# Optimization experiments

Hardware: AMD Instinct MI355X
Metric: run time of the kernel (lower is better)

## Reference

```python
import jax, jax.numpy as jnp
import numpy as np


def _conv(x, w, b=None, stride=1, pad=0, dil=1):
    out = jax.lax.conv_general_dilated(
        x, w, (stride, stride), [(pad, pad), (pad, pad)],
        rhs_dilation=(dil, dil),
        dimension_numbers=('NCHW', 'OIHW', 'NCHW'))
    return out if b is None else out + b[None, :, None, None]


def _sobel_base(out_ch, in_ch, k=3):
    # Exactly mirrors SobelConv2d weight construction (4 directional kernels).
    w = np.zeros((out_ch, in_ch, k, k), np.float32)
    m = k // 2
    for idx in range(out_ch):
        if idx % 4 == 0:
            w[idx, :, 0, :] = -1; w[idx, :, 0, m] = -2
            w[idx, :, -1, :] = 1; w[idx, :, -1, m] = 2
        elif idx % 4 == 1:
            w[idx, :, :, 0] = -1; w[idx, :, m, 0] = -2
            w[idx, :, :, -1] = 1; w[idx, :, m, -1] = 2
        elif idx % 4 == 2:
            w[idx, :, 0, 0] = -2
            for i in range(m + 1):
                w[idx, :, m - i, i] = -1
                w[idx, :, k - 1 - i, m + i] = 1
            w[idx, :, -1, -1] = 2
        else:
            w[idx, :, -1, 0] = -2
            for i in range(m + 1):
                w[idx, :, m + i, i] = -1
                w[idx, :, i, m + i] = 1
            w[idx, :, 0, -1] = 2
    return w


def setup_inputs() -> dict:
    key = jax.random.key(0)
    ks = iter(jax.random.split(key, 40))
    def p(shape, s=0.05):
        return jax.random.normal(next(ks), shape, dtype=jnp.float32) * s
    C = 32  # out_ch == sobel_ch
    f32 = jnp.float32
    return dict(
        x=jax.random.normal(next(ks), (8, 1, 256, 256), dtype=f32),
        sobel_base=jnp.asarray(_sobel_base(C, 1)),
        sobel_factor=jnp.ones((C, 1, 1, 1), f32),
        sobel_bias=jnp.zeros((C,), f32),
        f4_w=p((C, C + 1, 3, 3)), f4_b=jnp.zeros((C,), f32),
        ec1_w=p((C, C, 3, 3)), ec1_b=jnp.zeros((C,), f32),
        ec2_w=p((C, C, 3, 3)), ec2_b=jnp.zeros((C,), f32),
        ec3_w=p((C, C, 3, 3)), ec3_b=jnp.zeros((C,), f32),
        gate_w=p((3, 3 * C, 1, 1)), gate_b=jnp.zeros((3,), f32),
        ca1_w=p((C // 16, C, 1, 1)),  # ChannelAttention fc1 (ratio=16), no bias
        ca2_w=p((C, C // 16, 1, 1)),  # fc2, no bias
        sa_w=p((1, 2, 7, 7)),         # SpatialAttention conv, no bias
        p1_w=p((C, C, 1, 1)), p1_b=jnp.zeros((C,), f32),
        f1_w=p((C, C, 3, 3)), f1_b=jnp.zeros((C,), f32),
        p2_w=p((C, 2 * C, 1, 1)), p2_b=jnp.zeros((C,), f32),
        f2_w=p((C, C, 3, 3)), f2_b=jnp.zeros((C,), f32),
        p3_w=p((C, 2 * C, 1, 1)), p3_b=jnp.zeros((C,), f32),
        f3_w=p((C, C, 3, 3)), f3_b=jnp.zeros((C,), f32),
    )


def reference(x, sobel_base, sobel_factor, sobel_bias, f4_w, f4_b,
              ec1_w, ec1_b, ec2_w, ec2_b, ec3_w, ec3_b, gate_w, gate_b,
              ca1_w, ca2_w, sa_w,
              p1_w, p1_b, f1_w, f1_b, p2_w, p2_b, f2_w, f2_b,
              p3_w, p3_b, f3_w, f3_b):
    lrelu = lambda t: jax.nn.leaky_relu(t, 0.01)
    relu = jax.nn.relu
    # Sobel edge extraction (fixed directional kernels scaled by learned factor)
    out0 = _conv(x, sobel_base * sobel_factor, sobel_bias, pad=1)     # [B,32,H,W]
    out1 = jnp.concatenate([x, out0], axis=1)                          # [B,33,H,W]
    out1 = lrelu(_conv(out1, f4_w, f4_b, pad=1))                       # [B,32,H,W]
    # AdaptiveEdgeConnector: multi-dilation convs + softmax gating
    ex = relu(_conv(out1, ec1_w, ec1_b, pad=1))
    ey = relu(_conv(out1, ec2_w, ec2_b, pad=2, dil=2))
    ez = relu(_conv(out1, ec3_w, ec3_b, pad=3, dil=3))
    gates = jax.nn.softmax(_conv(jnp.concatenate([ex, ey, ez], axis=1), gate_w, gate_b), axis=1)
    enh = gates[:, 0:1] * ex + gates[:, 1:2] * ey + gates[:, 2:3] * ez
    # CBAM: channel attention
    avg = jnp.mean(enh, axis=(2, 3), keepdims=True)
    mx = jnp.max(enh, axis=(2, 3), keepdims=True)
    ca = jax.nn.sigmoid(_conv(relu(_conv(avg, ca1_w)), ca2_w)
                        + _conv(relu(_conv(mx, ca1_w)), ca2_w))
    f = ca * enh
    # CBAM: spatial attention
    sa_in = jnp.concatenate([jnp.mean(f, axis=1, keepdims=True),
                             jnp.max(f, axis=1, keepdims=True)], axis=1)
    sa = jax.nn.sigmoid(_conv(sa_in, sa_w, pad=3))
    edge = sa * f
    # Residual merge + cascaded dense conv stages
    out0 = lrelu(out1 + edge)
    t = lrelu(_conv(out0, p1_w, p1_b))
    t = lrelu(_conv(t, f1_w, f1_b, pad=1))
    o1 = jnp.concatenate([out0, t], axis=1)                            # [B,64,H,W]
    t = lrelu(_conv(o1, p2_w, p2_b))
    t = lrelu(_conv(t, f2_w, f2_b, pad=1))
    o2 = jnp.concatenate([out0, t], axis=1)
    t = lrelu(_conv(o2, p3_w, p3_b))
    t = lrelu(_conv(t, f3_w, f3_b, pad=1))
    return jnp.concatenate([out0, t], axis=1)                          # [B,64,H,W]
```

## Files before the change

### kernel.cpp

```cpp
#include <hip/hip_runtime.h>
#include <math.h>

typedef unsigned short u16;
typedef short short8 __attribute__((ext_vector_type(8)));
typedef float f32x4 __attribute__((ext_vector_type(4)));
typedef unsigned short ushort4v __attribute__((ext_vector_type(4)));

#define Hh 256
#define Ww 256
#define Bb 8
#define PW 262
#define PAD 3
#define HPW (Hh * PW)

__device__ __forceinline__ float bf2f(u16 v) {
    unsigned u = ((unsigned)v) << 16;
    union { unsigned u; float f; } c; c.u = u; return c.f;
}
__device__ __forceinline__ u16 f2bf(float f) {
    union { float f; unsigned u; } c; c.f = f;
    unsigned lsb = (c.u >> 16) & 1u;
    c.u += 0x7fffu + lsb;
    return (u16)(c.u >> 16);
}
__device__ __forceinline__ float sigm(float v) { return 1.f / (1.f + expf(-v)); }

template<int ACT, bool F32OUT, bool FUSEP>
__global__ __launch_bounds__(256) void convs_k(
    const u16* __restrict__ in, const u16* __restrict__ apack,
    const float* __restrict__ bias, void* __restrict__ outp,
    const u16* __restrict__ o0buf, const u16* __restrict__ pw,
    const float* __restrict__ pb, u16* __restrict__ pout)
{
    __shared__ u16 rows[4][4352];
    const int tid = threadIdx.x, lane = tid & 63, wv = tid >> 6;
    const int b = blockIdx.x & 7;
    const int rest = blockIdx.x >> 3;
    const int hpair = rest >> 1, half = rest & 1;
    const int h0 = hpair * 2;
    const int pl = wv * 32 + (lane & 15);
    const int icg = lane >> 4;

    for (int idx = tid; idx < 4 * 536; idx += 256) {
        int rr = idx / 536, q = idx % 536;
        int r = h0 - 1 + rr;
        short8 v = (short8){0, 0, 0, 0, 0, 0, 0, 0};
        if ((unsigned)r < 256u)
            v = *(const short8*)(in + ((size_t)b * HPW + (size_t)r * PW + PAD + half * 128 - 3) * 32
                                 + (size_t)q * 8);
        *(short8*)(&rows[rr][q * 8]) = v;
    }
    __syncthreads();

    f32x4 acc[2][2][2];
    #pragma unroll
    for (int r2 = 0; r2 < 2; ++r2)
        #pragma unroll
        for (int mf = 0; mf < 2; ++mf)
            #pragma unroll
            for (int nf = 0; nf < 2; ++nf)
                acc[r2][mf][nf] = (f32x4){0.f, 0.f, 0.f, 0.f};

    #pragma unroll
    for (int tap = 0; tap < 9; ++tap) {
        const int kh = tap / 3 - 1, kw = tap % 3 - 1;
        short8 a0 = *(const short8*)(apack + ((size_t)(tap * 2 + 0) * 64 + lane) * 8);
        short8 a1 = *(const short8*)(apack + ((size_t)(tap * 2 + 1) * 64 + lane) * 8);
        #pragma unroll
        for (int r2 = 0; r2 < 2; ++r2) {
            const int ri = 1 + r2 + kh;
            #pragma unroll
            for (int nf = 0; nf < 2; ++nf) {
                short8 bf = *(const short8*)(&rows[ri][(pl + nf * 16 + kw + 3) * 32 + icg * 8]);
                acc[r2][0][nf] = __builtin_amdgcn_mfma_f32_16x16x32_bf16(a0, bf, acc[r2][0][nf], 0, 0, 0);
                acc[r2][1][nf] = __builtin_amdgcn_mfma_f32_16x16x32_bf16(a1, bf, acc[r2][1][nf], 0, 0, 0);
            }
        }
    }
    const int nl = half * 128 + pl;
    f32x4 bi[2];
    bi[0] = *(const f32x4*)(bias + icg * 4);
    bi[1] = *(const f32x4*)(bias + 16 + icg * 4);

    if (FUSEP) {
        u16* tile = &rows[0][0];
        __syncthreads();
        #pragma unroll
        for (int r2 = 0; r2 < 2; ++r2)
            #pragma unroll
            for (int mf = 0; mf < 2; ++mf) {
                const int cob = mf * 16 + icg * 4;
                #pragma unroll
                for (int nf = 0; nf < 2; ++nf) {
                    ushort4v o;
                    #pragma unroll
                    for (int i = 0; i < 4; ++i) {
                        float v = acc[r2][mf][nf][i] + bi[mf][i];
                        v = (v > 0.f) ? v : 0.01f * v;
                        o[i] = f2bf(v);
                    }
                    *(ushort4v*)(tile + ((size_t)(r2 * 128 + pl + nf * 16)) * 32 + cob) = o;
                }
            }
        __syncthreads();
        #pragma unroll
        for (int r2 = 0; r2 < 2; ++r2) {
            const int h = h0 + r2;
            f32x4 acc2[2][2];
            #pragma unroll
            for (int mf = 0; mf < 2; ++mf)
                #pragma unroll
                for (int nf = 0; nf < 2; ++nf)
                    acc2[mf][nf] = (f32x4){0.f, 0.f, 0.f, 0.f};
            #pragma unroll
            for (int s = 0; s < 2; ++s) {
                short8 pa0 = *(const short8*)(pw + (size_t)(s * 2 + 0) * 512 + lane * 8);
                short8 pa1 = *(const short8*)(pw + (size_t)(s * 2 + 1) * 512 + lane * 8);
                #pragma unroll
                for (int nf = 0; nf < 2; ++nf) {
                    const int px = pl + nf * 16;
                    short8 bf;
                    if (s == 0)
                        bf = *(const short8*)(o0buf + ((size_t)b * HPW + (size_t)h * PW + PAD + half * 128 + px) * 32 + icg * 8);
                    else
                        bf = *(const short8*)(tile + ((size_t)(r2 * 128 + px)) * 32 + icg * 8);
                    acc2[0][nf] = __builtin_amdgcn_mfma_f32_16x16x32_bf16(pa0, bf, acc2[0][nf], 0, 0, 0);
                    acc2[1][nf] = __builtin_amdgcn_mfma_f32_16x16x32_bf16(pa1, bf, acc2[1][nf], 0, 0, 0);
                }
            }
            const size_t orow = ((size_t)b * HPW + (size_t)h * PW + PAD) * 32;
            #pragma unroll
            for (int mf = 0; mf < 2; ++mf) {
                const int cob = mf * 16 + icg * 4;
                f32x4 pbi = *(const f32x4*)(pb + cob);
                #pragma unroll
                for (int nf = 0; nf < 2; ++nf) {
                    ushort4v o;
                    #pragma unroll
                    for (int i = 0; i < 4; ++i) {
                        float v = acc2[mf][nf][i] + pbi[i];
                        v = (v > 0.f) ? v : 0.01f * v;
                        o[i] = f2bf(v);
                    }
                    *(ushort4v*)(pout + orow + (size_t)(nl + nf * 16) * 32 + cob) = o;
                }
            }
        }
        if (tid < 24) {
            int r2 = tid / 12, rem = tid % 12;
            int col3 = rem >> 2, chunk = rem & 3;
            int col = half ? (256 + PAD + col3) : col3;
            u16* pz = pout + ((size_t)b * HPW + (size_t)(h0 + r2) * PW + col) * 32 + chunk * 8;
            *(short8*)pz = (short8){0, 0, 0, 0, 0, 0, 0, 0};
        }
    } else if (F32OUT) {
        #pragma unroll
        for (int r2 = 0; r2 < 2; ++r2) {
            float* dp = (float*)outp + ((size_t)b * 64 + 32) * 65536 + (size_t)(h0 + r2) * 256;
            #pragma unroll
            for (int mf = 0; mf < 2; ++mf) {
                const int cob = mf * 16 + icg * 4;
                #pragma unroll
                for (int nf = 0; nf < 2; ++nf) {
                    const int w = nl + nf * 16;
                    #pragma unroll
                    for (int i = 0; i < 4; ++i) {
                        float v = acc[r2][mf][nf][i] + bi[mf][i];
                        if (ACT == 1) v = fmaxf(v, 0.f);
                        if (ACT == 2) v = (v > 0.f) ? v : 0.01f * v;
                        dp[(size_t)(cob + i) * 65536 + w] = v;
                    }
                }
            }
        }
    } else {
        u16* out = (u16*)outp;
        #pragma unroll
        for (int r2 = 0; r2 < 2; ++r2) {
            const size_t orow = ((size_t)b * HPW + (size_t)(h0 + r2) * PW + PAD) * 32;
            #pragma unroll
            for (int mf = 0; mf < 2; ++mf) {
                const int cob = mf * 16 + icg * 4;
                #pragma unroll
                for (int nf = 0; nf < 2; ++nf) {
                    ushort4v o;
                    #pragma unroll
                    for (int i = 0; i < 4; ++i) {
                        float v = acc[r2][mf][nf][i] + bi[mf][i];
                        if (ACT == 1) v = fmaxf(v, 0.f);
                        if (ACT == 2) v = (v > 0.f) ? v : 0.01f * v;
                        o[i] = f2bf(v);
                    }
                    *(ushort4v*)(out + orow + (size_t)(nl + nf * 16) * 32 + cob) = o;
                }
            }
        }
    }
}

__global__ __launch_bounds__(256) void ecfuse_k(
    const u16* __restrict__ in, const u16* __restrict__ apack,
    const float* __restrict__ b1, const float* __restrict__ b2,
    const float* __restrict__ b3, const float* __restrict__ gw_,
    const float* __restrict__ gb_, u16* __restrict__ enh)
{
    __shared__ u16 rows[3][4352];
    __shared__ float gw[288];
    __shared__ float gb[3];
    __shared__ float bs[96];
    int tid = threadIdx.x;
    for (int i = tid; i < 288; i += 256) gw[i] = gw_[i];
    if (tid < 3) gb[tid] = gb_[tid];
    if (tid < 32) bs[tid] = b1[tid];
    else if (tid < 64) bs[tid] = b2[tid - 32];
    else if (tid < 96) bs[tid] = b3[tid - 64];

    const int lane = tid & 63, wv = tid >> 6;
    const int b = blockIdx.x & 7;
    const int rest = blockIdx.x >> 3;
    const int h = rest >> 1, half = rest & 1;
    const int pl = wv * 32 + (lane & 15);
    const int icg = lane >> 4;

    f32x4 acc[3][2][2];
    #pragma unroll
    for (int cv = 0; cv < 3; ++cv)
        #pragma unroll
        for (int mf = 0; mf < 2; ++mf)
            #pragma unroll
            for (int nf = 0; nf < 2; ++nf)
                acc[cv][mf][nf] = (f32x4){0.f, 0.f, 0.f, 0.f};

    #pragma unroll
    for (int cv = 0; cv < 3; ++cv) {
        const int dil = cv + 1;
        __syncthreads();
        for (int idx = tid; idx < 3 * 536; idx += 256) {
            int rr = idx / 536, q = idx % 536;
            int r = h + (rr - 1) * dil;
            short8 v = (short8){0, 0, 0, 0, 0, 0, 0, 0};
            if ((unsigned)r < 256u)
                v = *(const short8*)(in + ((size_t)b * HPW + (size_t)r * PW + PAD + half * 128 - 3) * 32
                                     + (size_t)q * 8);
            *(short8*)(&rows[rr][q * 8]) = v;
        }
        __syncthreads();
        const u16* ap = apack + (size_t)(cv * 9 * 2) * 512;
        #pragma unroll
        for (int tap = 0; tap < 9; ++tap) {
            const int kh = tap / 3 - 1, kw = tap % 3 - 1;
            const int ri = 1 + kh;
            short8 a0 = *(const short8*)(ap + (size_t)(tap * 2 + 0) * 512 + lane * 8);
            short8 a1 = *(const short8*)(ap + (size_t)(tap * 2 + 1) * 512 + lane * 8);
            #pragma unroll
            for (int nf = 0; nf < 2; ++nf) {
                short8 bf = *(const short8*)(&rows[ri][(pl + nf * 16 + kw * dil + 3) * 32 + icg * 8]);
                acc[cv][0][nf] = __builtin_amdgcn_mfma_f32_16x16x32_bf16(a0, bf, acc[cv][0][nf], 0, 0, 0);
                acc[cv][1][nf] = __builtin_amdgcn_mfma_f32_16x16x32_bf16(a1, bf, acc[cv][1][nf], 0, 0, 0);
            }
        }
    }
    const int nl = half * 128 + pl;
    const size_t orow = ((size_t)b * HPW + (size_t)h * PW + PAD) * 32;
    #pragma unroll
    for (int nf = 0; nf < 2; ++nf) {
        float e[3][2][4];
        float g0 = 0.f, g1 = 0.f, g2 = 0.f;
        #pragma unroll
        for (int cv = 0; cv < 3; ++cv)
            #pragma unroll
            for (int mf = 0; mf < 2; ++mf) {
                const int cob = mf * 16 + icg * 4;
                #pragma unroll
                for (int i = 0; i < 4; ++i) {
                    float v = fmaxf(acc[cv][mf][nf][i] + bs[cv * 32 + cob + i], 0.f);
                    e[cv][mf][i] = v;
                    const int c = cv * 32 + cob + i;
                    g0 = fmaf(gw[c], v, g0);
                    g1 = fmaf(gw[96 + c], v, g1);
                    g2 = fmaf(gw[192 + c], v, g2);
                }
            }
        g0 += __shfl_xor(g0, 16); g0 += __shfl_xor(g0, 32);
        g1 += __shfl_xor(g1, 16); g1 += __shfl_xor(g1, 32);
        g2 += __shfl_xor(g2, 16); g2 += __shfl_xor(g2, 32);
        g0 += gb[0]; g1 += gb[1]; g2 += gb[2];
        float m = fmaxf(g0, fmaxf(g1, g2));
        float e0 = expf(g0 - m), e1 = expf(g1 - m), e2 = expf(g2 - m);
        float inv = 1.f / (e0 + e1 + e2);
        e0 *= inv; e1 *= inv; e2 *= inv;
        #pragma unroll
        for (int mf = 0; mf < 2; ++mf) {
            const int cob = mf * 16 + icg * 4;
            ushort4v o;
            #pragma unroll
            for (int i = 0; i < 4; ++i)
                o[i] = f2bf(e0 * e[0][mf][i] + e1 * e[1][mf][i] + e2 * e[2][mf][i]);
            *(ushort4v*)(enh + orow + (size_t)(nl + nf * 16) * 32 + cob) = o;
        }
    }
}

__global__ void prepack_k(
    const float* __restrict__ f4w, const float* __restrict__ e1w,
    const float* __restrict__ e2w, const float* __restrict__ e3w,
    const float* __restrict__ f1w, const float* __restrict__ f2w,
    const float* __restrict__ f3w, const float* __restrict__ p1w,
    const float* __restrict__ p2w, const float* __restrict__ p3w,
    u16* __restrict__ apack)
{
    int gid = blockIdx.x * 256 + threadIdx.x;
    if (gid >= 77 * 1024) return;
    const int offs[11] = {0, 18, 27, 36, 45, 54, 63, 72, 73, 75, 77};
    int step = gid >> 10, r = gid & 1023;
    int layer = 0;
    while (step >= offs[layer + 1]) layer++;
    int s = step - offs[layer];
    int mf = r >> 9, l = (r >> 3) & 63, j = r & 7;
    int co = mf * 16 + (l & 15);
    int ICB = (layer == 0 || layer == 8 || layer == 9) ? 2 : 1;
    int tap = s / ICB, icb = s % ICB;
    int icl = icb * 32 + (l >> 4) * 8 + j;
    float v = 0.f;
    if (layer == 0)      { if (icl < 33) v = f4w[(co * 33 + icl) * 9 + tap]; }
    else if (layer == 1) v = e1w[(co * 32 + icl) * 9 + tap];
    else if (layer == 2) v = e2w[(co * 32 + icl) * 9 + tap];
    else if (layer == 3) v = e3w[(co * 32 + icl) * 9 + tap];
    else if (layer == 4) v = f1w[(co * 32 + icl) * 9 + tap];
    else if (layer == 5) v = f2w[(co * 32 + icl) * 9 + tap];
    else if (layer == 6) v = f3w[(co * 32 + icl) * 9 + tap];
    else if (layer == 7) v = p1w[co * 32 + icl];
    else if (layer == 8) v = p2w[co * 64 + icl];
    else                 v = p3w[co * 64 + icl];
    apack[gid] = f2bf(v);
}

__global__ __launch_bounds__(256) void prep5_k(
    const float* __restrict__ f4w, const float* __restrict__ f4b,
    const float* __restrict__ sbase, const float* __restrict__ sfac,
    const float* __restrict__ sbias,
    float* __restrict__ w5, float* __restrict__ be)
{
    __shared__ float sF[32 * 33 * 9];
    __shared__ float sS[288];
    __shared__ float sBias[32];
    int t = threadIdx.x;
    for (int i = t; i < 32 * 33 * 9; i += 256) sF[i] = f4w[i];
    for (int i = t; i < 288; i += 256) sS[i] = sbase[i] * sfac[i / 9];
    if (t < 32) sBias[t] = sbias[t];
    __syncthreads();

    for (int idx = t; idx < 800; idx += 256) {
        int co = idx / 25, tap = idx % 25, kh = tap / 5, kw = tap % 5;
        float s = 0.f;
        if (kh >= 1 && kh <= 3 && kw >= 1 && kw <= 3)
            s = sF[(co * 33 + 0) * 9 + (kh - 1) * 3 + (kw - 1)];
        for (int sc = 0; sc < 32; ++sc) {
            #pragma unroll
            for (int a = 0; a < 3; ++a)
                #pragma unroll
                for (int bq = 0; bq < 3; ++bq) {
                    int p = kh - a, q = kw - bq;
                    if (p >= 0 && p < 3 && q >= 0 && q < 3)
                        s = fmaf(sF[(co * 33 + 1 + sc) * 9 + a * 3 + bq],
                                 sS[sc * 9 + p * 3 + q], s);
                }
        }
        w5[idx] = s;
    }
    for (int co = t; co < 32; co += 256) {
        float s = f4b[co];
        for (int sc = 0; sc < 32; ++sc) {
            float wsum = 0.f;
            #pragma unroll
            for (int k = 0; k < 9; ++k) wsum += sF[(co * 33 + 1 + sc) * 9 + k];
            s = fmaf(sBias[sc], wsum, s);
        }
        be[co] = s;
    }
}

__global__ __launch_bounds__(256) void conv5_k(
    const float* __restrict__ x, const float* __restrict__ w5,
    const float* __restrict__ be, u16* __restrict__ out1)
{
    __shared__ float sw[800];
    __shared__ float sb[32];
    int tid = threadIdx.x;
    for (int i = tid; i < 800; i += 256) sw[i] = w5[i];
    if (tid < 32) sb[tid] = be[tid];
    __syncthreads();
    int b = blockIdx.x & 7, h = blockIdx.x >> 3, w = tid;
    const float* xp = x + (size_t)b * 65536;
    float xv[25];
    #pragma unroll
    for (int i = 0; i < 5; ++i) {
        int r = h + i - 2;
        #pragma unroll
        for (int j = 0; j < 5; ++j) {
            int c = w + j - 2;
            xv[i * 5 + j] = ((unsigned)r < 256u && (unsigned)c < 256u)
                            ? xp[r * 256 + c] : 0.f;
        }
    }
    u16* dst = out1 + ((size_t)b * HPW + (size_t)h * PW + PAD + w) * 32;
    #pragma unroll
    for (int cb = 0; cb < 4; ++cb) {
        short8 o;
        #pragma unroll
        for (int j = 0; j < 8; ++j) {
            int co = cb * 8 + j;
            float s = sb[co];
            #pragma unroll
            for (int t2 = 0; t2 < 25; ++t2) s = fmaf(sw[co * 25 + t2], xv[t2], s);
            s = (s > 0.f) ? s : 0.01f * s;
            o[j] = (short)f2bf(s);
        }
        *(short8*)(dst + cb * 8) = o;
    }
    if (tid < 24) {
        int col6 = tid >> 2, chunk = tid & 3;
        int col = (col6 < 3) ? col6 : (256 + PAD + col6 - 3);
        u16* pz = out1 + ((size_t)b * HPW + (size_t)h * PW + col) * 32 + chunk * 8;
        *(short8*)pz = (short8){0, 0, 0, 0, 0, 0, 0, 0};
    }
}

__global__ __launch_bounds__(256) void ringfix_k(
    const float* __restrict__ x, const float* __restrict__ f4w,
    const float* __restrict__ f4b, const float* __restrict__ sbase,
    const float* __restrict__ sfac, const float* __restrict__ sbias,
    u16* __restrict__ out1)
{
    __shared__ float sW[288];
    __shared__ float sB[32];
    __shared__ float sF[32 * 33 * 9];
    __shared__ float sO[66][2][32];
    int tid = threadIdx.x;
    for (int i = tid; i < 288; i += 256) sW[i] = sbase[i] * sfac[i / 9];
    if (tid < 32) sB[tid] = sbias[tid];
    for (int i = tid; i < 32 * 33 * 9; i += 256) sF[i] = f4w[i];
    __syncthreads();

    int blk = blockIdx.x;
    int b = blk & 7, rest = blk >> 3;
    int e = rest >> 2, seg = rest & 3;
    const float* xp = x + (size_t)b * 65536;

    for (int i = tid; i < 66 * 2 * 32; i += 256) {
        int sc = i & 31, rr2 = i >> 5;
        int d = rr2 & 1, ul = rr2 >> 1;
        int ug = seg * 64 - 1 + ul;
        float v = 0.f;
        if ((unsigned)ug < 256u) {
            int h, w;
            if (e == 0)      { h = d;        w = ug; }
            else if (e == 1) { h = 255 - d;  w = ug; }
            else if (e == 2) { h = ug;       w = d; }
            else             { h = ug;       w = 255 - d; }
            float s = sB[sc];
            for (int p = 0; p < 3; ++p)
                for (int q = 0; q < 3; ++q) {
                    int rr = h + p - 1, cc = w + q - 1;
                    if ((unsigned)rr < 256u && (unsigned)cc < 256u)
                        s = fmaf(sW[sc * 9 + p * 3 + q], xp[rr * 256 + cc], s);
                }
            v = s;
        }
        sO[ul][d][sc] = v;
    }
    __syncthreads();

    int pi = tid & 63, cog = tid >> 6;
    int up = seg * 64 + pi;
    int h, w;
    if (e == 0)      { h = 0;   w = up; }
    else if (e == 1) { h = 255; w = up; }
    else if (e == 2) { h = up;  w = 0; }
    else             { h = up;  w = 255; }
    short8 ov;
    for (int cj = 0; cj < 8; ++cj) {
        int co = cog * 8 + cj;
        float acc = f4b[co];
        for (int a = 0; a < 3; ++a)
            for (int bb = 0; bb < 3; ++bb) {
                int hh = h + a - 1, ww = w + bb - 1;
                if ((unsigned)hh < 256u && (unsigned)ww < 256u)
                    acc = fmaf(sF[(co * 33) * 9 + a * 3 + bb], xp[hh * 256 + ww], acc);
                int d, ug;
                if (e == 0)      { d = hh;        ug = ww; }
                else if (e == 1) { d = 255 - hh;  ug = ww; }
                else if (e == 2) { d = ww;        ug = hh; }
                else             { d = 255 - ww;  ug = hh; }
                if (d >= 0 && d < 2 && (unsigned)ug < 256u) {
                    int ul = ug - (seg * 64 - 1);
                    for (int sc = 0; sc < 32; ++sc)
                        acc = fmaf(sF[(co * 33 + 1 + sc) * 9 + a * 3 + bb], sO[ul][d][sc], acc);
                }
            }
        acc = (acc > 0.f) ? acc : 0.01f * acc;
        ov[cj] = (short)f2bf(acc);
    }
    u16* dst = out1 + ((size_t)b * HPW + (size_t)h * PW + PAD + w) * 32 + cog * 8;
    *(short8*)dst = ov;
}

__global__ __launch_bounds__(256) void ca_part_k(
    const u16* __restrict__ enh, float* __restrict__ part)
{
    int blk = blockIdx.x, b = blk & 7, sl = blk >> 3;
    int tid = threadIdx.x, lane = tid & 63, wv = tid >> 6;
    float s[32], m[32];
    #pragma unroll
    for (int c = 0; c < 32; ++c) { s[c] = 0.f; m[c] = -1e30f; }
    for (int k = 0; k < 8; ++k) {
        int px = sl * 2048 + k * 256 + tid;
        int h = px >> 8, w = px & 255;
        size_t off = ((size_t)b * HPW + (size_t)h * PW + PAD + w) * 32;
        #pragma unroll
        for (int cb = 0; cb < 4; ++cb) {
            short8 v = *(const short8*)(enh + off + cb * 8);
            #pragma unroll
            for (int j = 0; j < 8; ++j) {
                float f = bf2f((u16)v[j]);
                s[cb * 8 + j] += f;
                m[cb * 8 + j] = fmaxf(m[cb * 8 + j], f);
            }
        }
    }
    #pragma unroll
    for (int c = 0; c < 32; ++c)
        #pragma unroll
        for (int o = 32; o; o >>= 1) {
            s[c] += __shfl_down(s[c], o);
            m[c] = fmaxf(m[c], __shfl_down(m[c], o));
        }
    __shared__ float ls[4][32], lm[4][32];
    if (lane == 0)
        for (int c = 0; c < 32; ++c) { ls[wv][c] = s[c]; lm[wv][c] = m[c]; }
    __syncthreads();
    if (tid < 32) {
        float ts = 0.f, tm = -1e30f;
        for (int w2 = 0; w2 < 4; ++w2) { ts += ls[w2][tid]; tm = fmaxf(tm, lm[w2][tid]); }
        int bs = b * 32 + sl;
        part[(size_t)(bs * 2 + 0) * 32 + tid] = ts;
        part[(size_t)(bs * 2 + 1) * 32 + tid] = tm;
    }
}

__global__ void ca_final_k(const float* __restrict__ part,
                           const float* __restrict__ w1, const float* __restrict__ w2,
                           float* __restrict__ ca)
{
    int t = threadIdx.x, b = t >> 5, c = t & 31;
    float s = 0.f, m = -1e30f;
    for (int sl = 0; sl < 32; ++sl) {
        int bs = b * 32 + sl;
        s += part[(size_t)(bs * 2 + 0) * 32 + c];
        m = fmaxf(m, part[(size_t)(bs * 2 + 1) * 32 + c]);
    }
    __shared__ float av[8][32], mx[8][32];
    av[b][c] = s * (1.f / 65536.f);
    mx[b][c] = m;
    __syncthreads();
    float sa0 = 0.f, sm0 = 0.f, sa1 = 0.f, sm1 = 0.f;
    for (int k = 0; k < 32; ++k) {
        float wa = w1[k], wb = w1[32 + k];
        sa0 = fmaf(wa, av[b][k], sa0); sm0 = fmaf(wa, mx[b][k], sm0);
        sa1 = fmaf(wb, av[b][k], sa1); sm1 = fmaf(wb, mx[b][k], sm1);
    }
    float h0 = fmaxf(sa0, 0.f) + fmaxf(sm0, 0.f);
    float h1 = fmaxf(sa1, 0.f) + fmaxf(sm1, 0.f);
    ca[t] = sigm(w2[c * 2 + 0] * h0 + w2[c * 2 + 1] * h1);
}

__global__ __launch_bounds__(256) void samap_k(
    const u16* __restrict__ enh, const float* __restrict__ ca,
    float* __restrict__ smap)
{
    __shared__ float sca[256];
    int tid = threadIdx.x;
    sca[tid] = ca[tid];
    __syncthreads();
    int b = blockIdx.x & 7;
    int r = (blockIdx.x >> 3) * 256 + tid;
    if (r >= 262 * 262) return;
    int ph = r / 262, pw = r % 262;
    float mean = 0.f, mxv = 0.f;
    if (ph >= 3 && ph < 259 && pw >= 3 && pw < 259) {
        int h = ph - 3, w = pw - 3;
        size_t off = ((size_t)b * HPW + (size_t)h * PW + PAD + w) * 32;
        float s = 0.f, m = -1e30f;
        #pragma unroll
        for (int cb = 0; cb < 4; ++cb) {
            short8 v = *(const short8*)(enh + off + cb * 8);
            #pragma unroll
            for (int j = 0; j < 8; ++j) {
                float f = bf2f((u16)v[j]) * sca[b * 32 + cb * 8 + j];
                s += f; m = fmaxf(m, f);
            }
        }
        mean = s * (1.f / 32.f); mxv = m;
    }
    smap[((size_t)b * 262 * 262 + (size_t)ph * 262 + pw) * 2 + 0] = mean;
    smap[((size_t)b * 262 * 262 + (size_t)ph * 262 + pw) * 2 + 1] = mxv;
}

__global__ __launch_bounds__(256) void merge_k(
    const float* __restrict__ smap, const float* __restrict__ saw,
    const float* __restrict__ ca, const u16* __restrict__ out1,
    const u16* __restrict__ enh, u16* __restrict__ o0,
    float* __restrict__ dout,
    const u16* __restrict__ ap1, const float* __restrict__ p1b,
    u16* __restrict__ p1out)
{
    __shared__ float sw[98];
    __shared__ float sca[256];
    __shared__ u16 tile[256 * 32];
    int tid = threadIdx.x;
    for (int i = tid; i < 98; i += 256) sw[i] = saw[i];
    sca[tid] = ca[tid];
    __syncthreads();
    int b = blockIdx.x & 7;
    int h = blockIdx.x >> 3;
    int w = tid;
    const float* sp = smap + (size_t)b * 262 * 262 * 2;
    float acc = 0.f;
    #pragma unroll
    for (int kh = 0; kh < 7; ++kh)
        #pragma unroll
        for (int kw = 0; kw < 7; ++kw) {
            const float* q = sp + ((size_t)(h + kh) * 262 + (w + kw)) * 2;
            acc = fmaf(q[0], sw[kh * 7 + kw], acc);
            acc = fmaf(q[1], sw[49 + kh * 7 + kw], acc);
        }
    float sa = sigm(acc);
    size_t off = ((size_t)b * HPW + (size_t)h * PW + PAD + w) * 32;
    float* dp = dout + (size_t)b * 64 * 65536 + (size_t)h * 256 + w;
    #pragma unroll
    for (int cb = 0; cb < 4; ++cb) {
        short8 ve = *(const short8*)(enh + off + cb * 8);
        short8 vo = *(const short8*)(out1 + off + cb * 8);
        short8 o;
        #pragma unroll
        for (int j = 0; j < 8; ++j) {
            float f = sca[b * 32 + cb * 8 + j] * bf2f((u16)ve[j]);
            float v = bf2f((u16)vo[j]) + sa * f;
            v = (v > 0.f) ? v : 0.01f * v;
            o[j] = (short)f2bf(v);
            dp[(size_t)(cb * 8 + j) * 65536] = v;
        }
        *(short8*)(o0 + off + cb * 8) = o;
        *(short8*)(&tile[w * 32 + cb * 8]) = o;
    }
    __syncthreads();
    const int lane = tid & 63, wv = tid >> 6;
    const int icg = lane >> 4, l15 = lane & 15;
    f32x4 acc1[2][4];
    #pragma unroll
    for (int mf = 0; mf < 2; ++mf)
        #pragma unroll
        for (int nf = 0; nf < 4; ++nf)
            acc1[mf][nf] = (f32x4){0.f, 0.f, 0.f, 0.f};
    short8 pa0 = *(const short8*)(ap1 + (size_t)0 * 512 + lane * 8);
    short8 pa1 = *(const short8*)(ap1 + (size_t)1 * 512 + lane * 8);
    #pragma unroll
    for (int nf = 0; nf < 4; ++nf) {
        short8 bf = *(const short8*)(&tile[(wv * 64 + l15 + nf * 16) * 32 + icg * 8]);
        acc1[0][nf] = __builtin_amdgcn_mfma_f32_16x16x32_bf16(pa0, bf, acc1[0][nf], 0, 0, 0);
        acc1[1][nf] = __builtin_amdgcn_mfma_f32_16x16x32_bf16(pa1, bf, acc1[1][nf], 0, 0, 0);
    }
    const size_t orow = ((size_t)b * HPW + (size_t)h * PW + PAD) * 32;
    #pragma unroll
    for (int mf = 0; mf < 2; ++mf) {
        const int cob = mf * 16 + icg * 4;
        f32x4 pbi = *(const f32x4*)(p1b + cob);
        #pragma unroll
        for (int nf = 0; nf < 4; ++nf) {
            const int px = wv * 64 + l15 + nf * 16;
            ushort4v o;
            #pragma unroll
            for (int i = 0; i < 4; ++i) {
                float v = acc1[mf][nf][i] + pbi[i];
                v = (v > 0.f) ? v : 0.01f * v;
                o[i] = f2bf(v);
            }
            *(ushort4v*)(p1out + orow + (size_t)px * 32 + cob) = o;
        }
    }
}

extern "C" void kernel_launch(void* const* d_in, const int* in_sizes, int n_in,
                              void* d_out, int out_size, void* d_ws, size_t ws_size,
                              hipStream_t stream)
{
    (void)in_sizes; (void)n_in; (void)out_size; (void)ws_size;
    const float* x        = (const float*)d_in[0];
    const float* sob_base = (const float*)d_in[1];
    const float* sob_fac  = (const float*)d_in[2];
    const float* sob_bias = (const float*)d_in[3];
    const float* f4_w = (const float*)d_in[4];   const float* f4_b = (const float*)d_in[5];
    const float* ec1_w = (const float*)d_in[6];  const float* ec1_b = (const float*)d_in[7];
    const float* ec2_w = (const float*)d_in[8];  const float* ec2_b = (const float*)d_in[9];
    const float* ec3_w = (const float*)d_in[10]; const float* ec3_b = (const float*)d_in[11];
    const float* gate_w = (const float*)d_in[12]; const float* gate_b = (const float*)d_in[13];
    const float* ca1_w = (const float*)d_in[14]; const float* ca2_w = (const float*)d_in[15];
    const float* sa_w  = (const float*)d_in[16];
    const float* p1_w = (const float*)d_in[17]; const float* p1_b = (const float*)d_in[18];
    const float* f1_w = (const float*)d_in[19]; const float* f1_b = (const float*)d_in[20];
    const float* p2_w = (const float*)d_in[21]; const float* p2_b = (const float*)d_in[22];
    const float* f2_w = (const float*)d_in[23]; const float* f2_b = (const float*)d_in[24];
    const float* p3_w = (const float*)d_in[25]; const float* p3_b = (const float*)d_in[26];
    const float* f3_w = (const float*)d_in[27]; const float* f3_b = (const float*)d_in[28];

    const size_t PB32 = (size_t)Bb * HPW * 32 * 2;
    char* ws = (char*)d_ws;
    u16* Q    = (u16*)(ws);
    u16* O0   = (u16*)(ws + PB32);
    u16* T    = (u16*)(ws + 2 * PB32);
    u16* ENH  = (u16*)(ws + 3 * PB32);
    u16* AP   = (u16*)(ws + 4 * PB32);
    float* W5   = (float*)(ws + 4 * PB32 + 77 * 1024 * 2);
    float* BE   = W5 + 800;
    float* PART = BE + 32;
    float* CA   = PART + 8 * 32 * 2 * 32;

    char* doutc = (char*)d_out;
    float* SMAP = (float*)(doutc + (134217728 - (size_t)Bb * 262 * 262 * 2 * 4));
    float* dout = (float*)d_out;

    dim3 blk(256);

    prepack_k<<<308, blk, 0, stream>>>(f4_w, ec1_w, ec2_w, ec3_w, f1_w, f2_w, f3_w,
                                       p1_w, p2_w, p3_w, AP);
    prep5_k<<<1, blk, 0, stream>>>(f4_w, f4_b, sob_base, sob_fac, sob_bias, W5, BE);
    conv5_k<<<2048, blk, 0, stream>>>(x, W5, BE, Q);
    ringfix_k<<<128, blk, 0, stream>>>(x, f4_w, f4_b, sob_base, sob_fac, sob_bias, Q);
    ecfuse_k<<<4096, blk, 0, stream>>>(Q, AP + 18 * 1024, ec1_b, ec2_b, ec3_b,
                                       gate_w, gate_b, ENH);
    ca_part_k<<<256, blk, 0, stream>>>(ENH, PART);
    ca_final_k<<<1, blk, 0, stream>>>(PART, ca1_w, ca2_w, CA);
    samap_k<<<2152, blk, 0, stream>>>(ENH, CA, SMAP);
    merge_k<<<2048, blk, 0, stream>>>(SMAP, sa_w, CA, Q, ENH, O0, dout,
                                      AP + 72 * 1024, p1_b, Q);
    convs_k<2, false, true ><<<2048, blk, 0, stream>>>(Q, AP + 45 * 1024, f1_b, nullptr,
                                                       O0, AP + 73 * 1024, p2_b, T);
    convs_k<2, false, true ><<<2048, blk, 0, stream>>>(T, AP + 54 * 1024, f2_b, nullptr,
                                                       O0, AP + 75 * 1024, p3_b, Q);
    convs_k<2, true, false><<<2048, blk, 0, stream>>>(Q, AP + 63 * 1024, f3_b, dout,
                                                      nullptr, nullptr, nullptr, nullptr);
}
```

Measured before the change: 399.2 us.

## Double-buffer dilated row tiles in ecfuse kernel to overlap global loads with MFMA

The ecfuse kernel now keeps two LDS buffers of three input rows. While the MFMA taps for one dilation run, the rows for the next dilation are prefetched from global memory into registers and written to the other buffer afterwards. This takes the global-load latency off the path between dilation stages and drops one barrier per stage. In exchange it roughly doubles LDS use and holds six extra short8 registers per thread, which may reduce occupancy.

```diff
diff --git a/kernel.cpp b/kernel.cpp
--- a/kernel.cpp
+++ b/kernel.cpp
@@ -204,7 +204,7 @@
     const float* __restrict__ b3, const float* __restrict__ gw_,
     const float* __restrict__ gb_, u16* __restrict__ enh)
 {
-    __shared__ u16 rows[3][4352];
+    __shared__ u16 rows[2][3][4288];
     __shared__ float gw[288];
     __shared__ float gb[3];
     __shared__ float bs[96];
@@ -221,6 +221,17 @@
     const int h = rest >> 1, half = rest & 1;
     const int pl = wv * 32 + (lane & 15);
     const int icg = lane >> 4;
+    const u16* src_base = in + ((size_t)b * HPW + PAD + half * 128 - 3) * 32;
+
+    for (int idx = tid; idx < 1608; idx += 256) {
+        int rr = idx / 536, q = idx % 536;
+        int r = h + (rr - 1);
+        short8 v = (short8){0, 0, 0, 0, 0, 0, 0, 0};
+        if ((unsigned)r < 256u)
+            v = *(const short8*)(src_base + (size_t)r * PW * 32 + (size_t)q * 8);
+        *(short8*)(&rows[0][rr][q * 8]) = v;
+    }
+    __syncthreads();
 
     f32x4 acc[3][2][2];
     #pragma unroll
@@ -234,17 +245,23 @@
     #pragma unroll
     for (int cv = 0; cv < 3; ++cv) {
         const int dil = cv + 1;
-        __syncthreads();
-        for (int idx = tid; idx < 3 * 536; idx += 256) {
-            int rr = idx / 536, q = idx % 536;
-            int r = h + (rr - 1) * dil;
-            short8 v = (short8){0, 0, 0, 0, 0, 0, 0, 0};
-            if ((unsigned)r < 256u)
-                v = *(const short8*)(in + ((size_t)b * HPW + (size_t)r * PW + PAD + half * 128 - 3) * 32
-                                     + (size_t)q * 8);
-            *(short8*)(&rows[rr][q * 8]) = v;
-        }
-        __syncthreads();
+        const int nb = cv & 1;
+        short8 stg0, stg1, stg2, stg3, stg4, stg5;
+        if (cv < 2) {
+            const int dn = cv + 2;
+            #pragma unroll
+            for (int k = 0; k < 6; ++k) {
+                int idx = tid + k * 256;
+                int rr = idx / 536, q = idx % 536;
+                int r = h + (rr - 1) * dn;
+                short8 v = (short8){0, 0, 0, 0, 0, 0, 0, 0};
+                if ((unsigned)r < 256u)
+                    v = *(const short8*)(src_base + (size_t)r * PW * 32 + (size_t)q * 8);
+                if (k == 0) stg0 = v; else if (k == 1) stg1 = v;
+                else if (k == 2) stg2 = v; else if (k == 3) stg3 = v;
+                else if (k == 4) stg4 = v; else stg5 = v;
+            }
+        }
         const u16* ap = apack + (size_t)(cv * 9 * 2) * 512;
         #pragma unroll
         for (int tap = 0; tap < 9; ++tap) {
@@ -254,10 +271,31 @@
             short8 a1 = *(const short8*)(ap + (size_t)(tap * 2 + 1) * 512 + lane * 8);
             #pragma unroll
             for (int nf = 0; nf < 2; ++nf) {
-                short8 bf = *(const short8*)(&rows[ri][(pl + nf * 16 + kw * dil + 3) * 32 + icg * 8]);
+                short8 bf = *(const short8*)(&rows[nb][ri][(pl + nf * 16 + kw * dil + 3) * 32 + icg * 8]);
                 acc[cv][0][nf] = __builtin_amdgcn_mfma_f32_16x16x32_bf16(a0, bf, acc[cv][0][nf], 0, 0, 0);
                 acc[cv][1][nf] = __builtin_amdgcn_mfma_f32_16x16x32_bf16(a1, bf, acc[cv][1][nf], 0, 0, 0);
             }
+        }
+        if (cv < 2) {
+            const int dn = cv + 2;
+            #pragma unroll
+            for (int k = 0; k < 6; ++k) {
+                int idx = tid + k * 256;
+                int rr = idx / 536, q = idx % 536;
+                short8 v = (k == 0) ? stg0 : (k == 1) ? stg1 : (k == 2) ? stg2
+                         : (k == 3) ? stg3 : (k == 4) ? stg4 : stg5;
+                *(short8*)(&rows[1 - nb][rr][q * 8]) = v;
+            }
+            if (tid < 72) {
+                int idx = tid + 1536;
+                int rr = idx / 536, q = idx % 536;
+                int r = h + (rr - 1) * dn;
+                short8 v = (short8){0, 0, 0, 0, 0, 0, 0, 0};
+                if ((unsigned)r < 256u)
+                    v = *(const short8*)(src_base + (size_t)r * PW * 32 + (size_t)q * 8);
+                *(short8*)(&rows[1 - nb][rr][q * 8]) = v;
+            }
+            __syncthreads();
         }
     }
     const int nl = half * 128 + pl;
```

Result: faster. 389.7 us (-2.4%).
